# Kernel optimization log

Hardware: AMD Instinct MI355X
Metric: run time of the kernel (lower is better)

Reference implementation:

```python
import jax, jax.numpy as jnp
import numpy as np

N_NODES = 50000
N_EDGES = 800000
N_FEAT = 64
HIDDEN = 64
N_GRAPHS = 64
N_CLASSES = 10
BN_EPS = 1e-5


def setup_inputs() -> dict:
    key = jax.random.key(0)
    ks = jax.random.split(key, 12)
    x = jax.random.normal(ks[0], (N_NODES, N_FEAT), dtype=jnp.float32)
    edge_index = jax.random.randint(ks[1], (2, N_EDGES), 0, N_NODES, dtype=jnp.int64)
    # equal-sized, sorted graph assignment so every graph is non-empty for max-pool
    batch = (jnp.arange(N_NODES, dtype=jnp.int64) * N_GRAPHS) // N_NODES
    s = 0.1
    return {
        "x": x,
        "edge_index": edge_index,
        "batch": batch,
        "W1": jax.random.normal(ks[2], (N_FEAT, HIDDEN), jnp.float32) * s,
        "b1": jnp.zeros((HIDDEN,), jnp.float32),
        "W2": jax.random.normal(ks[3], (HIDDEN, HIDDEN), jnp.float32) * s,
        "b2": jnp.zeros((HIDDEN,), jnp.float32),
        "W3": jax.random.normal(ks[4], (HIDDEN, HIDDEN), jnp.float32) * s,
        "b3": jnp.zeros((HIDDEN,), jnp.float32),
        # NOTE: source uses [Norm(hidden)]*3 -> ONE shared BatchNorm across layers
        "gamma": jnp.ones((HIDDEN,), jnp.float32),
        "beta": jnp.zeros((HIDDEN,), jnp.float32),
        "lin1_w": jax.random.normal(ks[5], (HIDDEN, HIDDEN), jnp.float32) * s,
        "lin1_b": jnp.zeros((HIDDEN,), jnp.float32),
        "lin2_w": jax.random.normal(ks[6], (HIDDEN, N_CLASSES), jnp.float32) * s,
        "lin2_b": jnp.zeros((N_CLASSES,), jnp.float32),
    }


def reference(x, edge_index, batch, W1, b1, W2, b2, W3, b3, gamma, beta,
              lin1_w, lin1_b, lin2_w, lin2_b):
    N = x.shape[0]
    src, dst = edge_index[0], edge_index[1]
    # GCN symmetric normalization with self-loops: deg = in-degree + 1
    deg = jax.ops.segment_sum(jnp.ones(src.shape[0], x.dtype), dst, num_segments=N) + 1.0
    dis = jax.lax.rsqrt(deg)                      # [N]
    coef = (dis[src] * dis[dst])[:, None]         # [E,1] edge norm
    self_coef = (dis * dis)[:, None]              # [N,1] self-loop norm

    def gcn_conv(h, W, b):
        h = h @ W                                  # [N,H] tiny GEMM
        agg = jax.ops.segment_sum(h[src] * coef, dst, num_segments=N)
        return agg + h * self_coef + b

    def batch_norm(h):
        mu = h.mean(axis=0)
        var = h.var(axis=0)                        # biased var, torch BN training mode
        return gamma * (h - mu) * jax.lax.rsqrt(var + BN_EPS) + beta

    out = x
    for W, b in ((W1, b1), (W2, b2), (W3, b3)):
        out = jax.nn.relu(batch_norm(gcn_conv(out, W, b)))

    emb = jax.ops.segment_max(out, batch, num_segments=N_GRAPHS)  # global_max_pool
    return jax.nn.relu(emb @ lin1_w + lin1_b) @ lin2_w + lin2_b
```

## Files before the change

### kernel.cpp

```cpp
#include <hip/hip_runtime.h>
#include <hip/hip_bf16.h>

#define N_NODES 50000
#define N_EDGES 800000
#define HID 64
#define N_GRAPHS 64
#define N_CLASSES 10
#define BN_EPS 1e-5f
#define NPART 196
#define FILL_BLOCKS 128

typedef unsigned int uint;
typedef unsigned short ushort;

__device__ __forceinline__ float blo(uint u) { return __uint_as_float(u << 16); }
__device__ __forceinline__ float bhi(uint u) { return __uint_as_float(u & 0xffff0000u); }
__device__ __forceinline__ unsigned short f2b(float f) {
  __hip_bfloat16 h = __float2bfloat16(f);
  return *reinterpret_cast<unsigned short*>(&h);
}


__global__ void k_zero_small(int* __restrict__ p, int n) {
  int i = threadIdx.x;
  if (i < n) p[i] = 0;
}

__global__ __launch_bounds__(256) void k_hist(const int* __restrict__ dst,
                                              int* __restrict__ ghist) {
  __shared__ int l[NPART];
  int tid = threadIdx.x;
  for (int i = tid; i < NPART; i += 256) l[i] = 0;
  __syncthreads();
  const int per = (N_EDGES + FILL_BLOCKS - 1) / FILL_BLOCKS;
  int c0 = blockIdx.x * per;
  int c1 = c0 + per;
  if (c1 > N_EDGES) c1 = N_EDGES;
  for (int e = c0 + tid; e < c1; e += 256)
    atomicAdd(&l[__builtin_nontemporal_load(&dst[e]) >> 8], 1);
  __syncthreads();
  for (int p = tid; p < NPART; p += 256)
    if (l[p]) atomicAdd(&ghist[p], l[p]);
}

__global__ void k_scan196(const int* __restrict__ ghist, int* __restrict__ bro,
                          int* __restrict__ pcur, int* __restrict__ rowp) {
  __shared__ int s[256];
  int tid = threadIdx.x;
  int v = (tid < NPART) ? ghist[tid] : 0;
  s[tid] = v;
  __syncthreads();
  for (int off = 1; off < 256; off <<= 1) {
    int t = (tid >= off) ? s[tid - off] : 0;
    __syncthreads();
    s[tid] += t;
    __syncthreads();
  }
  if (tid < NPART) {
    int e = s[tid] - v;
    bro[tid] = e;
    pcur[tid] = e;
  }
  if (tid == 0) {
    bro[NPART] = N_EDGES;
    rowp[N_NODES] = N_EDGES;
  }
}

__global__ __launch_bounds__(256) void k_partA(const int* __restrict__ ei,
                                               int* __restrict__ pcur,
                                               uint* __restrict__ tmp) {
  __shared__ int lcnt[NPART];
  __shared__ int lbase[NPART];
  int tid = threadIdx.x;
  const int per = (N_EDGES + FILL_BLOCKS - 1) / FILL_BLOCKS;
  int c0 = blockIdx.x * per;
  int c1 = c0 + per;
  if (c1 > N_EDGES) c1 = N_EDGES;
  for (int i = tid; i < NPART; i += 256) lcnt[i] = 0;
  __syncthreads();
  for (int e = c0 + tid; e < c1; e += 256) {
    int d = __builtin_nontemporal_load(&ei[N_EDGES + e]);
    atomicAdd(&lcnt[d >> 8], 1);
  }
  __syncthreads();
  for (int p = tid; p < NPART; p += 256) lbase[p] = atomicAdd(&pcur[p], lcnt[p]);
  __syncthreads();
  for (int e = c0 + tid; e < c1; e += 256) {
    int s = __builtin_nontemporal_load(&ei[e]);
    int d = __builtin_nontemporal_load(&ei[N_EDGES + e]);
    int pos = atomicAdd(&lbase[d >> 8], 1);
    tmp[pos] = ((uint)s << 8) | (uint)(d & 255);
  }
}

__global__ __launch_bounds__(256) void k_partB(const uint* __restrict__ tmp,
                                               const int* __restrict__ bro,
                                               float* __restrict__ dis,
                                               int* __restrict__ rowp,
                                               ushort* __restrict__ eus) {
  __shared__ int cnt[256];
  __shared__ int s[256];
  __shared__ int cur[256];
  int tid = threadIdx.x;
  int p = blockIdx.x;
  int base = bro[p], pend = bro[p + 1];
  cnt[tid] = 0;
  __syncthreads();
  for (int idx = base + tid; idx < pend; idx += 256)
    atomicAdd(&cnt[__builtin_nontemporal_load(&tmp[idx]) & 255u], 1);
  __syncthreads();
  int deg = cnt[tid];
  int n = (p << 8) + tid;
  if (n < N_NODES) dis[n] = rsqrtf((float)deg + 1.0f);
  s[tid] = deg;
  __syncthreads();
  for (int off = 1; off < 256; off <<= 1) {
    int t = (tid >= off) ? s[tid - off] : 0;
    __syncthreads();
    s[tid] += t;
    __syncthreads();
  }
  int start = base + s[tid] - deg;
  if (n < N_NODES) rowp[n] = start;
  cur[tid] = start;
  __syncthreads();
  for (int idx = base + tid; idx < pend; idx += 256) {
    uint t = __builtin_nontemporal_load(&tmp[idx]);
    int pos = atomicAdd(&cur[t & 255u], 1);
    eus[pos] = (ushort)(t >> 8);
  }
}


template <bool IN_BF16>
__global__ __launch_bounds__(256) void k_gemm(const void* __restrict__ in,
                                              const float* __restrict__ W,
                                              __hip_bfloat16* __restrict__ out,
                                              float* __restrict__ stats_zero,
                                              const float* __restrict__ stats_in,
                                              const float* __restrict__ gamma,
                                              const float* __restrict__ beta) {
  __shared__ float Al[4][64];
  int tid = threadIdx.x;
  int wid = tid >> 6, f = tid & 63;
  if (blockIdx.x == 0) {
    for (int i = tid; i < 1024; i += 256) stats_zero[i] = 0.0f;
  }
  float Wreg[64];
#pragma unroll
  for (int k = 0; k < 64; ++k) Wreg[k] = W[k * 64 + f];
  float sc = 1.f, sh = 0.f;
  if (stats_in) {
    float s = 0.f, q = 0.f;
#pragma unroll
    for (int c = 0; c < 8; ++c) {
      s += stats_in[c * 128 + f];
      q += stats_in[c * 128 + 64 + f];
    }
    float mu = s * (1.0f / N_NODES);
    float var = q * (1.0f / N_NODES) - mu * mu;
    sc = gamma[f] * rsqrtf(var + BN_EPS);
    sh = beta[f] - mu * sc;
  }
  for (int n = blockIdx.x * 4 + wid; n < N_NODES; n += gridDim.x * 4) {
    float av;
    if (IN_BF16) {
      ushort u = ((const ushort*)in)[(n << 6) + f];
      av = __uint_as_float((uint)u << 16);
    } else {
      av = ((const float*)in)[(n << 6) + f];
    }
    if (stats_in) {
      av = fmaf(av, sc, sh);
      av = av > 0.f ? av : 0.f;
    }
    Al[wid][f] = av;
    float acc = 0.f;
    const float4* arow = (const float4*)Al[wid];
#pragma unroll
    for (int k4 = 0; k4 < 16; ++k4) {
      float4 a = arow[k4];
      acc = fmaf(a.x, Wreg[k4 * 4 + 0], acc);
      acc = fmaf(a.y, Wreg[k4 * 4 + 1], acc);
      acc = fmaf(a.z, Wreg[k4 * 4 + 2], acc);
      acc = fmaf(a.w, Wreg[k4 * 4 + 3], acc);
    }
    out[(n << 6) + f] = __float2bfloat16(acc);
  }
}

__global__ __launch_bounds__(256, 4) void k_agg_node(
    const __hip_bfloat16* __restrict__ hW, const float* __restrict__ dis,
    const int* __restrict__ rowp, const ushort* __restrict__ eus,
    const float* __restrict__ bias, __hip_bfloat16* __restrict__ act,
    float* __restrict__ stats) {
  __shared__ float sstat[4][2][64];
  int tid = threadIdx.x;
  int wid = tid >> 6, lane = tid & 63;
  int g = lane >> 3, l8 = lane & 7;
  int n = (blockIdx.x * 4 + wid) * 8 + g;
  const uint4* hw4 = (const uint4*)hW;
  float pre[8] = {0, 0, 0, 0, 0, 0, 0, 0};
  float sq[8] = {0, 0, 0, 0, 0, 0, 0, 0};
  if (n < N_NODES) {
    int p0 = rowp[n], p1 = rowp[n + 1];
    float dn = dis[n];
    float acc[8] = {0, 0, 0, 0, 0, 0, 0, 0};
    for (int pb = p0; pb < p1; pb += 8) {
      int idx = pb + l8;
      if (idx >= N_EDGES) idx = N_EDGES - 1;
      uint rs = eus[idx];
#pragma unroll
      for (int h = 0; h < 2; ++h) {
        uint e4[4];
        float ds4[4];
        uint4 hv[4];
#pragma unroll
        for (int u = 0; u < 4; ++u) e4[u] = __shfl(rs, (g << 3) | (h * 4 + u), 64);
#pragma unroll
        for (int u = 0; u < 4; ++u) {
          hv[u] = hw4[e4[u] * 8 + l8];
          ds4[u] = dis[e4[u]];
        }
#pragma unroll
        for (int u = 0; u < 4; ++u) {
          float wv = (pb + h * 4 + u < p1) ? ds4[u] * dn : 0.f;
          acc[0] = fmaf(blo(hv[u].x), wv, acc[0]);
          acc[1] = fmaf(bhi(hv[u].x), wv, acc[1]);
          acc[2] = fmaf(blo(hv[u].y), wv, acc[2]);
          acc[3] = fmaf(bhi(hv[u].y), wv, acc[3]);
          acc[4] = fmaf(blo(hv[u].z), wv, acc[4]);
          acc[5] = fmaf(bhi(hv[u].z), wv, acc[5]);
          acc[6] = fmaf(blo(hv[u].w), wv, acc[6]);
          acc[7] = fmaf(bhi(hv[u].w), wv, acc[7]);
        }
      }
    }
    float dn2 = dn * dn;
    uint4 hs = hw4[n * 8 + l8];
    const float4* b4 = (const float4*)bias;
    float4 bA = b4[l8 * 2], bB = b4[l8 * 2 + 1];
    pre[0] = fmaf(blo(hs.x), dn2, acc[0]) + bA.x;
    pre[1] = fmaf(bhi(hs.x), dn2, acc[1]) + bA.y;
    pre[2] = fmaf(blo(hs.y), dn2, acc[2]) + bA.z;
    pre[3] = fmaf(bhi(hs.y), dn2, acc[3]) + bA.w;
    pre[4] = fmaf(blo(hs.z), dn2, acc[4]) + bB.x;
    pre[5] = fmaf(bhi(hs.z), dn2, acc[5]) + bB.y;
    pre[6] = fmaf(blo(hs.w), dn2, acc[6]) + bB.z;
    pre[7] = fmaf(bhi(hs.w), dn2, acc[7]) + bB.w;
    uint4 st;
    st.x = (uint)f2b(pre[0]) | ((uint)f2b(pre[1]) << 16);
    st.y = (uint)f2b(pre[2]) | ((uint)f2b(pre[3]) << 16);
    st.z = (uint)f2b(pre[4]) | ((uint)f2b(pre[5]) << 16);
    st.w = (uint)f2b(pre[6]) | ((uint)f2b(pre[7]) << 16);
    ((uint4*)act)[n * 8 + l8] = st;
#pragma unroll
    for (int i = 0; i < 8; ++i) sq[i] = pre[i] * pre[i];
  }
#pragma unroll
  for (int off = 8; off < 64; off <<= 1) {
#pragma unroll
    for (int i = 0; i < 8; ++i) {
      pre[i] += __shfl_xor(pre[i], off, 64);
      sq[i] += __shfl_xor(sq[i], off, 64);
    }
  }
  if (g == 0) {
#pragma unroll
    for (int i = 0; i < 8; ++i) {
      sstat[wid][0][l8 * 8 + i] = pre[i];
      sstat[wid][1][l8 * 8 + i] = sq[i];
    }
  }
  __syncthreads();
  if (tid < 128) {
    int which = tid >> 6, f = tid & 63;
    float s = sstat[0][which][f] + sstat[1][which][f] + sstat[2][which][f] +
              sstat[3][which][f];
    atomicAdd(&stats[(blockIdx.x & 7) * 128 + which * 64 + f], s);
  }
}


__global__ __launch_bounds__(256) void k_pool(const __hip_bfloat16* __restrict__ act,
                                              const float* __restrict__ stats_in,
                                              const float* __restrict__ gamma,
                                              const float* __restrict__ beta,
                                              float* __restrict__ pooled) {
  int g = blockIdx.x;
  int tid = threadIdx.x;
  int l16 = tid & 15;
  int r = tid >> 4;
  float sc[4], sh[4];
#pragma unroll
  for (int i = 0; i < 4; ++i) {
    int f = l16 * 4 + i;
    float s = 0.f, q = 0.f;
#pragma unroll
    for (int c = 0; c < 8; ++c) {
      s += stats_in[c * 128 + f];
      q += stats_in[c * 128 + 64 + f];
    }
    float mu = s * (1.0f / N_NODES);
    float var = q * (1.0f / N_NODES) - mu * mu;
    sc[i] = gamma[f] * rsqrtf(var + BN_EPS);
    sh[i] = beta[f] - mu * sc[i];
  }
  int gs = g * N_NODES;
  int start = (gs + 63) >> 6;
  int end = (gs + N_NODES + 63) >> 6;
  float m[4] = {0.f, 0.f, 0.f, 0.f};
  const uint2* a2 = (const uint2*)act;
  for (int n = start + r; n < end; n += 16) {
    uint2 v = a2[n * 16 + l16];
    m[0] = fmaxf(m[0], fmaf(blo(v.x), sc[0], sh[0]));
    m[1] = fmaxf(m[1], fmaf(bhi(v.x), sc[1], sh[1]));
    m[2] = fmaxf(m[2], fmaf(blo(v.y), sc[2], sh[2]));
    m[3] = fmaxf(m[3], fmaf(bhi(v.y), sc[3], sh[3]));
  }
  __shared__ float sm[16][64];
#pragma unroll
  for (int i = 0; i < 4; ++i) sm[r][l16 * 4 + i] = m[i];
  __syncthreads();
  if (tid < 64) {
    float mm = sm[0][tid];
#pragma unroll
    for (int rr = 1; rr < 16; ++rr) mm = fmaxf(mm, sm[rr][tid]);
    pooled[g * 64 + tid] = mm;
  }
}

__global__ __launch_bounds__(256) void k_final(const float* __restrict__ pooled,
                                               const float* __restrict__ w1,
                                               const float* __restrict__ b1,
                                               const float* __restrict__ w2,
                                               const float* __restrict__ b2,
                                               float* __restrict__ out) {
  __shared__ float P[64 * 64];
  __shared__ float Hd[64 * 64];
  int tid = threadIdx.x;
  for (int i = tid; i < 4096; i += 256) P[i] = pooled[i];
  __syncthreads();
  for (int i = tid; i < 4096; i += 256) {
    int g = i >> 6, j = i & 63;
    float acc = b1[j];
#pragma unroll
    for (int k = 0; k < 64; ++k) acc = fmaf(P[g * 64 + k], w1[k * 64 + j], acc);
    Hd[i] = acc > 0.f ? acc : 0.f;
  }
  __syncthreads();
  for (int i = tid; i < 640; i += 256) {
    int g = i / 10, c = i % 10;
    float acc = b2[c];
#pragma unroll
    for (int k = 0; k < 64; ++k) acc = fmaf(Hd[g * 64 + k], w2[k * 10 + c], acc);
    out[i] = acc;
  }
}


extern "C" void kernel_launch(void* const* d_in, const int* in_sizes, int n_in,
                              void* d_out, int out_size, void* d_ws, size_t ws_size,
                              hipStream_t stream) {
  const float* x = (const float*)d_in[0];
  const int* ei = (const int*)d_in[1];
  const float* W1 = (const float*)d_in[3];
  const float* b1 = (const float*)d_in[4];
  const float* W2 = (const float*)d_in[5];
  const float* b2 = (const float*)d_in[6];
  const float* W3 = (const float*)d_in[7];
  const float* b3 = (const float*)d_in[8];
  const float* gamma = (const float*)d_in[9];
  const float* beta = (const float*)d_in[10];
  const float* l1w = (const float*)d_in[11];
  const float* l1b = (const float*)d_in[12];
  const float* l2w = (const float*)d_in[13];
  const float* l2b = (const float*)d_in[14];
  float* out = (float*)d_out;

  char* ws = (char*)d_ws;
  size_t off = 0;
  auto alloc = [&](size_t bytes) {
    void* p = ws + off;
    off = (off + bytes + 255) & ~(size_t)255;
    return p;
  };
  int* ghist = (int*)alloc(NPART * 4);
  int* bro = (int*)alloc((NPART + 1) * 4);
  int* pcur = (int*)alloc(NPART * 4);
  int* rowp = (int*)alloc((N_NODES + 1) * 4);
  uint* tmp = (uint*)alloc((size_t)N_EDGES * 4);
  ushort* eus = (ushort*)alloc((size_t)N_EDGES * 2 + 512);
  float* dis = (float*)alloc(N_NODES * 4);
  __hip_bfloat16* hW = (__hip_bfloat16*)alloc((size_t)N_NODES * 64 * 2);
  __hip_bfloat16* act = (__hip_bfloat16*)alloc((size_t)N_NODES * 64 * 2);
  float* statsL0 = (float*)alloc(1024 * 4);
  float* statsL1 = (float*)alloc(1024 * 4);
  float* statsL2 = (float*)alloc(1024 * 4);
  float* pooled = (float*)alloc(4096 * 4);

  int nag = (N_NODES + 31) / 32;

  k_zero_small<<<1, 256, 0, stream>>>(ghist, NPART);
  k_hist<<<FILL_BLOCKS, 256, 0, stream>>>(ei + N_EDGES, ghist);
  k_scan196<<<1, 256, 0, stream>>>(ghist, bro, pcur, rowp);
  k_partA<<<FILL_BLOCKS, 256, 0, stream>>>(ei, pcur, tmp);
  k_partB<<<NPART, 256, 0, stream>>>(tmp, bro, dis, rowp, eus);

  k_gemm<false><<<2048, 256, 0, stream>>>(x, W1, hW, statsL0, nullptr, gamma, beta);
  k_agg_node<<<nag, 256, 0, stream>>>(hW, dis, rowp, eus, b1, act, statsL0);
  k_gemm<true><<<2048, 256, 0, stream>>>(act, W2, hW, statsL1, statsL0, gamma, beta);
  k_agg_node<<<nag, 256, 0, stream>>>(hW, dis, rowp, eus, b2, act, statsL1);
  k_gemm<true><<<2048, 256, 0, stream>>>(act, W3, hW, statsL2, statsL1, gamma, beta);
  k_agg_node<<<nag, 256, 0, stream>>>(hW, dis, rowp, eus, b3, act, statsL2);

  k_pool<<<N_GRAPHS, 256, 0, stream>>>(act, statsL2, gamma, beta, pooled);
  k_final<<<1, 256, 0, stream>>>(pooled, l1w, l1b, l2w, l2b, out);
}
```

Baseline: 201.6 us.

## Split feature arrays into two 32-column halves to shrink gather working set

Hidden and activation arrays are stored as two separate 32-feature halves (A/B). The aggregation kernel now runs each block on one half, with 4 lanes per node and 16 nodes per wave. Blocks are interleaved so that blocks handling the same node range for both halves sit close together. The goal is to make each random gather pass touch a 3.2MB table instead of 6.4MB, so it fits better in L2/cache. The cost is that each node's edge list, degree scales and row pointers are read twice. The GEMM and pool kernels are adapted to the split layout.

Result: slower. 215.9 us (+7.1%).

```diff
diff --git a/kernel.cpp b/kernel.cpp
--- a/kernel.cpp
+++ b/kernel.cpp
@@ -134,9 +134,11 @@
 
 
 template <bool IN_BF16>
-__global__ __launch_bounds__(256) void k_gemm(const void* __restrict__ in,
+__global__ __launch_bounds__(256) void k_gemm(const void* __restrict__ inA,
+                                              const void* __restrict__ inB,
                                               const float* __restrict__ W,
-                                              __hip_bfloat16* __restrict__ out,
+                                              __hip_bfloat16* __restrict__ outA,
+                                              __hip_bfloat16* __restrict__ outB,
                                               float* __restrict__ stats_zero,
                                               const float* __restrict__ stats_in,
                                               const float* __restrict__ gamma,
@@ -163,13 +165,16 @@
     sc = gamma[f] * rsqrtf(var + BN_EPS);
     sh = beta[f] - mu * sc;
   }
+  const ushort* inH = (const ushort*)((f < 32) ? inA : inB);
+  __hip_bfloat16* outH = (f < 32) ? outA : outB;
+  int fh = f & 31;
   for (int n = blockIdx.x * 4 + wid; n < N_NODES; n += gridDim.x * 4) {
     float av;
     if (IN_BF16) {
-      ushort u = ((const ushort*)in)[(n << 6) + f];
+      ushort u = inH[(n << 5) + fh];
       av = __uint_as_float((uint)u << 16);
     } else {
-      av = ((const float*)in)[(n << 6) + f];
+      av = ((const float*)inA)[(n << 6) + f];
     }
     if (stats_in) {
       av = fmaf(av, sc, sh);
@@ -186,41 +191,50 @@
       acc = fmaf(a.z, Wreg[k4 * 4 + 2], acc);
       acc = fmaf(a.w, Wreg[k4 * 4 + 3], acc);
     }
-    out[(n << 6) + f] = __float2bfloat16(acc);
-  }
-}
-
-__global__ __launch_bounds__(256, 4) void k_agg_node(
-    const __hip_bfloat16* __restrict__ hW, const float* __restrict__ dis,
-    const int* __restrict__ rowp, const ushort* __restrict__ eus,
-    const float* __restrict__ bias, __hip_bfloat16* __restrict__ act,
+    outH[(n << 5) + fh] = __float2bfloat16(acc);
+  }
+}
+
+__global__ __launch_bounds__(256, 4) void k_agg2(
+    const __hip_bfloat16* __restrict__ hA, const __hip_bfloat16* __restrict__ hB,
+    const float* __restrict__ dis, const int* __restrict__ rowp,
+    const ushort* __restrict__ eus, const float* __restrict__ bias,
+    __hip_bfloat16* __restrict__ actA, __hip_bfloat16* __restrict__ actB,
     float* __restrict__ stats) {
-  __shared__ float sstat[4][2][64];
+  __shared__ float sstat[4][2][32];
   int tid = threadIdx.x;
   int wid = tid >> 6, lane = tid & 63;
-  int g = lane >> 3, l8 = lane & 7;
-  int n = (blockIdx.x * 4 + wid) * 8 + g;
-  const uint4* hw4 = (const uint4*)hW;
+  int g16 = lane >> 2, l4 = lane & 3;
+  int b = blockIdx.x;
+  int xg = b & 7;
+  int pass = (xg >= 4) ? 1 : 0;
+  int rank = (b >> 3) * 4 + (xg & 3);
+  const uint4* hw4 = (const uint4*)(pass ? hB : hA);
+  __hip_bfloat16* actH = pass ? actB : actA;
+  int n = (rank * 4 + wid) * 16 + g16;
   float pre[8] = {0, 0, 0, 0, 0, 0, 0, 0};
   float sq[8] = {0, 0, 0, 0, 0, 0, 0, 0};
   if (n < N_NODES) {
     int p0 = rowp[n], p1 = rowp[n + 1];
     float dn = dis[n];
+    uint4 hs = hw4[n * 4 + l4];
     float acc[8] = {0, 0, 0, 0, 0, 0, 0, 0};
     for (int pb = p0; pb < p1; pb += 8) {
-      int idx = pb + l8;
-      if (idx >= N_EDGES) idx = N_EDGES - 1;
-      uint rs = eus[idx];
+      int i0 = pb + l4;
+      int i1 = pb + 4 + l4;
+      uint r0 = (i0 < p1) ? (uint)eus[i0] : 0u;
+      uint r1 = (i1 < p1) ? (uint)eus[i1] : 0u;
 #pragma unroll
       for (int h = 0; h < 2; ++h) {
         uint e4[4];
         float ds4[4];
         uint4 hv[4];
-#pragma unroll
-        for (int u = 0; u < 4; ++u) e4[u] = __shfl(rs, (g << 3) | (h * 4 + u), 64);
+        uint rr = h ? r1 : r0;
+#pragma unroll
+        for (int u = 0; u < 4; ++u) e4[u] = __shfl(rr, (g16 << 2) | u, 64);
 #pragma unroll
         for (int u = 0; u < 4; ++u) {
-          hv[u] = hw4[e4[u] * 8 + l8];
+          hv[u] = hw4[e4[u] * 4 + l4];
           ds4[u] = dis[e4[u]];
         }
 #pragma unroll
@@ -238,9 +252,8 @@
       }
     }
     float dn2 = dn * dn;
-    uint4 hs = hw4[n * 8 + l8];
-    const float4* b4 = (const float4*)bias;
-    float4 bA = b4[l8 * 2], bB = b4[l8 * 2 + 1];
+    const float4* b4 = (const float4*)(bias + pass * 32);
+    float4 bA = b4[l4 * 2], bB = b4[l4 * 2 + 1];
     pre[0] = fmaf(blo(hs.x), dn2, acc[0]) + bA.x;
     pre[1] = fmaf(bhi(hs.x), dn2, acc[1]) + bA.y;
     pre[2] = fmaf(blo(hs.y), dn2, acc[2]) + bA.z;
@@ -254,36 +267,37 @@
     st.y = (uint)f2b(pre[2]) | ((uint)f2b(pre[3]) << 16);
     st.z = (uint)f2b(pre[4]) | ((uint)f2b(pre[5]) << 16);
     st.w = (uint)f2b(pre[6]) | ((uint)f2b(pre[7]) << 16);
-    ((uint4*)act)[n * 8 + l8] = st;
+    ((uint4*)actH)[n * 4 + l4] = st;
 #pragma unroll
     for (int i = 0; i < 8; ++i) sq[i] = pre[i] * pre[i];
   }
 #pragma unroll
-  for (int off = 8; off < 64; off <<= 1) {
+  for (int off = 4; off < 64; off <<= 1) {
 #pragma unroll
     for (int i = 0; i < 8; ++i) {
       pre[i] += __shfl_xor(pre[i], off, 64);
       sq[i] += __shfl_xor(sq[i], off, 64);
     }
   }
-  if (g == 0) {
+  if (g16 == 0) {
 #pragma unroll
     for (int i = 0; i < 8; ++i) {
-      sstat[wid][0][l8 * 8 + i] = pre[i];
-      sstat[wid][1][l8 * 8 + i] = sq[i];
-    }
-  }
-  __syncthreads();
-  if (tid < 128) {
-    int which = tid >> 6, f = tid & 63;
+      sstat[wid][0][l4 * 8 + i] = pre[i];
+      sstat[wid][1][l4 * 8 + i] = sq[i];
+    }
+  }
+  __syncthreads();
+  if (tid < 64) {
+    int which = tid >> 5, f = tid & 31;
     float s = sstat[0][which][f] + sstat[1][which][f] + sstat[2][which][f] +
               sstat[3][which][f];
-    atomicAdd(&stats[(blockIdx.x & 7) * 128 + which * 64 + f], s);
-  }
-}
-
-
-__global__ __launch_bounds__(256) void k_pool(const __hip_bfloat16* __restrict__ act,
+    atomicAdd(&stats[(b & 7) * 128 + which * 64 + pass * 32 + f], s);
+  }
+}
+
+
+__global__ __launch_bounds__(256) void k_pool(const __hip_bfloat16* __restrict__ actA,
+                                              const __hip_bfloat16* __restrict__ actB,
                                               const float* __restrict__ stats_in,
                                               const float* __restrict__ gamma,
                                               const float* __restrict__ beta,
@@ -307,13 +321,14 @@
     sc[i] = gamma[f] * rsqrtf(var + BN_EPS);
     sh[i] = beta[f] - mu * sc[i];
   }
+  const uint2* src = (l16 < 8) ? (const uint2*)actA : (const uint2*)actB;
+  int chunk = l16 & 7;
   int gs = g * N_NODES;
   int start = (gs + 63) >> 6;
   int end = (gs + N_NODES + 63) >> 6;
   float m[4] = {0.f, 0.f, 0.f, 0.f};
-  const uint2* a2 = (const uint2*)act;
   for (int n = start + r; n < end; n += 16) {
-    uint2 v = a2[n * 16 + l16];
+    uint2 v = src[n * 8 + chunk];
     m[0] = fmaxf(m[0], fmaf(blo(v.x), sc[0], sh[0]));
     m[1] = fmaxf(m[1], fmaf(bhi(v.x), sc[1], sh[1]));
     m[2] = fmaxf(m[2], fmaf(blo(v.y), sc[2], sh[2]));
@@ -393,14 +408,16 @@
   uint* tmp = (uint*)alloc((size_t)N_EDGES * 4);
   ushort* eus = (ushort*)alloc((size_t)N_EDGES * 2 + 512);
   float* dis = (float*)alloc(N_NODES * 4);
-  __hip_bfloat16* hW = (__hip_bfloat16*)alloc((size_t)N_NODES * 64 * 2);
-  __hip_bfloat16* act = (__hip_bfloat16*)alloc((size_t)N_NODES * 64 * 2);
+  __hip_bfloat16* hA = (__hip_bfloat16*)alloc((size_t)N_NODES * 32 * 2);
+  __hip_bfloat16* hB = (__hip_bfloat16*)alloc((size_t)N_NODES * 32 * 2);
+  __hip_bfloat16* actA = (__hip_bfloat16*)alloc((size_t)N_NODES * 32 * 2);
+  __hip_bfloat16* actB = (__hip_bfloat16*)alloc((size_t)N_NODES * 32 * 2);
   float* statsL0 = (float*)alloc(1024 * 4);
   float* statsL1 = (float*)alloc(1024 * 4);
   float* statsL2 = (float*)alloc(1024 * 4);
   float* pooled = (float*)alloc(4096 * 4);
 
-  int nag = (N_NODES + 31) / 32;
+  int nag = NPART * 8;
 
   k_zero_small<<<1, 256, 0, stream>>>(ghist, NPART);
   k_hist<<<FILL_BLOCKS, 256, 0, stream>>>(ei + N_EDGES, ghist);
@@ -408,13 +425,13 @@
   k_partA<<<FILL_BLOCKS, 256, 0, stream>>>(ei, pcur, tmp);
   k_partB<<<NPART, 256, 0, stream>>>(tmp, bro, dis, rowp, eus);
 
-  k_gemm<false><<<2048, 256, 0, stream>>>(x, W1, hW, statsL0, nullptr, gamma, beta);
-  k_agg_node<<<nag, 256, 0, stream>>>(hW, dis, rowp, eus, b1, act, statsL0);
-  k_gemm<true><<<2048, 256, 0, stream>>>(act, W2, hW, statsL1, statsL0, gamma, beta);
-  k_agg_node<<<nag, 256, 0, stream>>>(hW, dis, rowp, eus, b2, act, statsL1);
-  k_gemm<true><<<2048, 256, 0, stream>>>(act, W3, hW, statsL2, statsL1, gamma, beta);
-  k_agg_node<<<nag, 256, 0, stream>>>(hW, dis, rowp, eus, b3, act, statsL2);
-
-  k_pool<<<N_GRAPHS, 256, 0, stream>>>(act, statsL2, gamma, beta, pooled);
+  k_gemm<false><<<2048, 256, 0, stream>>>(x, nullptr, W1, hA, hB, statsL0, nullptr, gamma, beta);
+  k_agg2<<<nag, 256, 0, stream>>>(hA, hB, dis, rowp, eus, b1, actA, actB, statsL0);
+  k_gemm<true><<<2048, 256, 0, stream>>>(actA, actB, W2, hA, hB, statsL1, statsL0, gamma, beta);
+  k_agg2<<<nag, 256, 0, stream>>>(hA, hB, dis, rowp, eus, b2, actA, actB, statsL1);
+  k_gemm<true><<<2048, 256, 0, stream>>>(actA, actB, W3, hA, hB, statsL2, statsL1, gamma, beta);
+  k_agg2<<<nag, 256, 0, stream>>>(hA, hB, dis, rowp, eus, b3, actA, actB, statsL2);
+
+  k_pool<<<N_GRAPHS, 256, 0, stream>>>(actA, actB, statsL2, gamma, beta, pooled);
   k_final<<<1, 256, 0, stream>>>(pooled, l1w, l1b, l2w, l2b, out);
 }
```
